# Optimization experiments

Hardware: AMD Instinct MI355X
Metric: run time of the kernel (lower is better)

Reference implementation:

```python
import jax, jax.numpy as jnp
import numpy as np

ITERATIONS = 5


def _dilate3x3(x):
    # 3x3 box 'conv' with all-ones kernel, padding=1 (SAME), single channel, NCHW
    k = jnp.ones((1, 1, 3, 3), x.dtype)
    return jax.lax.conv_general_dilated(
        x, k, window_strides=(1, 1), padding='SAME',
        dimension_numbers=('NCHW', 'OIHW', 'NCHW'))


def setup_inputs() -> dict:
    key = jax.random.key(0)
    k1, k2 = jax.random.split(key)
    H = W = 4096
    prediction = jax.random.uniform(k1, (1, 1, H, W), dtype=jnp.float32)
    ground_truth = jax.random.uniform(k2, (1, 1, H, W), dtype=jnp.float32)
    return {"prediction": prediction, "ground_truth": ground_truth}


def reference(prediction, ground_truth):
    # distance_weight = [1, 4, 9, 16, 25]
    weights = jnp.asarray([(i + 1) ** 2 for i in range(ITERATIONS)], dtype=jnp.float32)
    gt_sum = jnp.sum(ground_truth)
    fn_total = jnp.zeros((), dtype=jnp.float32)
    pred = prediction
    for i in range(ITERATIONS):  # fixed small unrolled loop (sequential recurrence)
        dilated = jnp.clip(_dilate3x3(pred), 0.0, 1.0)
        sharp = jax.nn.sigmoid(20.0 * (dilated - pred - 0.5))
        false_negative = ground_truth * sharp
        fn_total = fn_total + weights[i] * jnp.sum(false_negative) / gt_sum
        pred = pred + false_negative  # fed into next iteration's dilation
    return fn_total
```

## Files before the change

### kernel.cpp

```cpp
#include <hip/hip_runtime.h>

#define N 4096
#define CORE_W 116
#define NSTRIP 36
#define ROWS 36
#define NCHUNK 114
#define NSLOT 32
#define WPB 4
#define NBLOCK ((NSTRIP * NCHUNK) / WPB)


typedef float2 f2;
__device__ __forceinline__ f2 mkf2(float a, float b){ f2 r; r.x=a; r.y=b; return r; }

__device__ __forceinline__ f2 hsum(f2 v) {
    float m = v.x + v.y;
    float L = __shfl_up(v.y, 1);
    float R = __shfl_down(v.x, 1);
    return mkf2(L + m, m + R);
}

__device__ __forceinline__ f2 stepf(f2 p, f2 d, f2 g, f2* fn) {
    const float C1 = 28.853900817779268f;
    const float C2 = 14.426950408889634f;
    f2 o, f;
    {
        float dd = fminf(fmaxf(d.x, 0.f), 1.f);
        float u  = __builtin_fmaf(p.x - dd, C1, C2);
        float sh = __builtin_amdgcn_rcpf(1.f + __builtin_amdgcn_exp2f(u));
        f.x = g.x * sh; o.x = p.x + f.x;
    }
    {
        float dd = fminf(fmaxf(d.y, 0.f), 1.f);
        float u  = __builtin_fmaf(p.y - dd, C1, C2);
        float sh = __builtin_amdgcn_rcpf(1.f + __builtin_amdgcn_exp2f(u));
        f.y = g.y * sh; o.y = p.y + f.y;
    }
    *fn = f;
    return o;
}

__device__ __forceinline__ f2 ldrow(const float* __restrict__ base, int row,
                                    int gc, bool edge) {
    if (row < 0 || row >= N) return mkf2(0.f, 0.f);
    if (!edge) return *(const f2*)(base + (size_t)row * N + gc);
    float a = 0.f, b = 0.f;
    if (gc >= 0 && gc < N)         a = base[(size_t)row * N + gc];
    if (gc + 1 >= 0 && gc + 1 < N) b = base[(size_t)row * N + gc + 1];
    return mkf2(a, b);
}

__global__ __launch_bounds__(64 * WPB, 4) void wlc_main(
    const float* __restrict__ pred,
    const float* __restrict__ gt,
    float* __restrict__ ws)
{
    const int lane   = threadIdx.x & 63;
    const int wid    = threadIdx.x >> 6;
    const int linear = blockIdx.x * WPB + wid;
    const int strip  = linear % NSTRIP;
    const int chunk  = linear / NSTRIP;
    const int x0 = strip * CORE_W - 6;
    const int gc = x0 + 2 * lane;
    const bool edge = (strip == 0) || (strip == NSTRIP - 1);

    const int R0 = chunk * ROWS;
    const int R1 = min(R0 + ROWS, N);
    const int t0 = R0 - 5;
    const int t1 = R1 + 5;

    const float colm = (lane >= 3 && lane <= 60) ? 1.f : 0.f;
    const float m0 = (gc     < N) ? colm : 0.f;
    const float m1 = (gc + 1 < N) ? colm : 0.f;

    f2 pr[6], gb[6];
    f2 hp0, hp1, hp2, hp3, hp4;
    f2 ps0, ps1, ps2, ps3, ps4;
    f2 o1[2], o2[2], o3[2], o4[2];
#pragma unroll
    for (int i = 0; i < 6; ++i) { pr[i] = mkf2(0,0); gb[i] = mkf2(0,0); }
    hp0=hp1=hp2=hp3=hp4=mkf2(0,0);
    ps0=ps1=ps2=ps3=ps4=mkf2(0,0);
#pragma unroll
    for (int i = 0; i < 2; ++i) { o1[i]=o2[i]=o3[i]=o4[i]=mkf2(0,0); }

    pr[2] = ldrow(pred, t0,     gc, edge);
    pr[3] = ldrow(pred, t0 + 1, gc, edge);

    f2 swv = mkf2(0.f, 0.f);
    f2 gsv = mkf2(0.f, 0.f);

#define S6(o) ((8 + k + (o)) % 6)
#define S2(o) ((8 + k + (o)) % 2)

    for (int tb = t0; tb < t1; tb += 6) {
#pragma unroll
        for (int k = 0; k < 6; ++k) {
            const int t = tb + k;
            if (t < t1) {
                const f2 g5 = gb[S6(-5)];
                if (t + 2 <= R1 + 4) pr[S6(2)] = ldrow(pred, t + 2, gc, edge);
                if (t + 1 <= R1 + 3) gb[S6(1)] = ldrow(gt,   t + 1, gc, edge);

                const float w1 = (t-1 >= R0 && t-1 < R1) ? 1.f  : 0.f;
                const float w2 = (t-2 >= R0 && t-2 < R1) ? 4.f  : 0.f;
                const float w3 = (t-3 >= R0 && t-3 < R1) ? 9.f  : 0.f;
                const float w4 = (t-4 >= R0 && t-4 < R1) ? 16.f : 0.f;
                const bool  in5 = (t-5 >= R0 && t-5 < R1);
                const float w5 = in5 ? 25.f : 0.f;
                const float g1 = in5 ? 1.f  : 0.f;

                f2 hn, d, fn, o;

                hn = hsum(pr[S6(0)]);
                d  = mkf2(hn.x + ps0.x, hn.y + ps0.y);
                ps0 = mkf2(hn.x + hp0.x, hn.y + hp0.y);
                hp0 = hn;

                o = stepf(pr[S6(-1)], d, gb[S6(-1)], &fn);
                swv.x = __builtin_fmaf(w1, fn.x, swv.x);
                swv.y = __builtin_fmaf(w1, fn.y, swv.y);
                hn = hsum(o);  o1[S2(-1)] = o;
                d  = mkf2(hn.x + ps1.x, hn.y + ps1.y);
                ps1 = mkf2(hn.x + hp1.x, hn.y + hp1.y);
                hp1 = hn;

                o = stepf(o1[S2(-2)], d, gb[S6(-2)], &fn);
                swv.x = __builtin_fmaf(w2, fn.x, swv.x);
                swv.y = __builtin_fmaf(w2, fn.y, swv.y);
                hn = hsum(o);  o2[S2(-2)] = o;
                d  = mkf2(hn.x + ps2.x, hn.y + ps2.y);
                ps2 = mkf2(hn.x + hp2.x, hn.y + hp2.y);
                hp2 = hn;

                o = stepf(o2[S2(-3)], d, gb[S6(-3)], &fn);
                swv.x = __builtin_fmaf(w3, fn.x, swv.x);
                swv.y = __builtin_fmaf(w3, fn.y, swv.y);
                hn = hsum(o);  o3[S2(-3)] = o;
                d  = mkf2(hn.x + ps3.x, hn.y + ps3.y);
                ps3 = mkf2(hn.x + hp3.x, hn.y + hp3.y);
                hp3 = hn;

                o = stepf(o3[S2(-4)], d, gb[S6(-4)], &fn);
                swv.x = __builtin_fmaf(w4, fn.x, swv.x);
                swv.y = __builtin_fmaf(w4, fn.y, swv.y);
                hn = hsum(o);  o4[S2(-4)] = o;
                d  = mkf2(hn.x + ps4.x, hn.y + ps4.y);
                ps4 = mkf2(hn.x + hp4.x, hn.y + hp4.y);
                hp4 = hn;

                o = stepf(o4[S2(-5)], d, g5, &fn);
                swv.x = __builtin_fmaf(w5, fn.x, swv.x);
                swv.y = __builtin_fmaf(w5, fn.y, swv.y);
                gsv.x = __builtin_fmaf(g1, g5.x, gsv.x);
                gsv.y = __builtin_fmaf(g1, g5.y, gsv.y);
            }
        }
    }
#undef S6
#undef S2

    float vals[2];
    vals[0] = gsv.x * m0 + gsv.y * m1;
    vals[1] = swv.x * m0 + swv.y * m1;
    const int slot = (strip + chunk * NSTRIP) & (NSLOT - 1);
#pragma unroll
    for (int kk = 0; kk < 2; ++kk) {
        float v = vals[kk];
#pragma unroll
        for (int off = 32; off > 0; off >>= 1)
            v += __shfl_down(v, off, 64);
        if (lane == 0) atomicAdd(&ws[slot * 32 + kk], v);
    }
}

__global__ __launch_bounds__(64) void wlc_final(const float* __restrict__ ws,
                                                float* __restrict__ out)
{
    const int lane = threadIdx.x;
    float t0 = (lane < NSLOT) ? ws[lane * 32 + 0] : 0.f;
    float t1 = (lane < NSLOT) ? ws[lane * 32 + 1] : 0.f;
#pragma unroll
    for (int off = 32; off > 0; off >>= 1) {
        t0 += __shfl_down(t0, off, 64);
        t1 += __shfl_down(t1, off, 64);
    }
    if (lane == 0)
        out[0] = t1 / t0;
}

extern "C" void kernel_launch(void* const* d_in, const int* in_sizes, int n_in,
                              void* d_out, int out_size, void* d_ws, size_t ws_size,
                              hipStream_t stream)
{
    const float* pred = (const float*)d_in[0];
    const float* gtp  = (const float*)d_in[1];
    float* ws = (float*)d_ws;

    hipMemsetAsync(d_ws, 0, NSLOT * 32 * sizeof(float), stream);

    wlc_main<<<dim3(NBLOCK), 64 * WPB, 0, stream>>>(pred, gtp, ws);
    wlc_final<<<1, 64, 0, stream>>>(ws, (float*)d_out);
}
```

Before: 189.7 us.

## Skew stencil pipeline stages to break dependency chains and use larger row chunks

Restructures the five-iteration streaming stencil so that alternate stages lag by an extra row. Those stages can then compute their vertical sums from stored ring buffers instead of waiting on the stage just before them in the same row, which shortens the serial dependency chain per row. A second ground-truth stream is loaded at an offset to feed the delayed stages. Row chunks grow from 36 to 74 to amortise halo recompute, and the launch moves to single-wave blocks on a 2D grid. The cost is more registers, an extra gt load per row, and fewer waves in total (2016 vs 4104).

```diff
diff --git a/kernel.cpp b/kernel.cpp
--- a/kernel.cpp
+++ b/kernel.cpp
@@ -3,11 +3,9 @@
 #define N 4096
 #define CORE_W 116
 #define NSTRIP 36
-#define ROWS 36
-#define NCHUNK 114
+#define ROWS 74
+#define NCHUNK 56
 #define NSLOT 32
-#define WPB 4
-#define NBLOCK ((NSTRIP * NCHUNK) / WPB)
 
 
 typedef float2 f2;
@@ -50,115 +48,123 @@
     return mkf2(a, b);
 }
 
-__global__ __launch_bounds__(64 * WPB, 4) void wlc_main(
+__global__ __launch_bounds__(64, 2) void wlc_main(
     const float* __restrict__ pred,
     const float* __restrict__ gt,
     float* __restrict__ ws)
 {
-    const int lane   = threadIdx.x & 63;
-    const int wid    = threadIdx.x >> 6;
-    const int linear = blockIdx.x * WPB + wid;
-    const int strip  = linear % NSTRIP;
-    const int chunk  = linear / NSTRIP;
+    const int lane  = threadIdx.x;
+    const int strip = blockIdx.x;
+    const int chunk = blockIdx.y;
     const int x0 = strip * CORE_W - 6;
     const int gc = x0 + 2 * lane;
     const bool edge = (strip == 0) || (strip == NSTRIP - 1);
 
     const int R0 = chunk * ROWS;
     const int R1 = min(R0 + ROWS, N);
-    const int t0 = R0 - 5;
-    const int t1 = R1 + 5;
+    const int t0 = R0 - 6;
+    const int jmax = (R1 - R0) + 13;
 
     const float colm = (lane >= 3 && lane <= 60) ? 1.f : 0.f;
     const float m0 = (gc     < N) ? colm : 0.f;
     const float m1 = (gc + 1 < N) ? colm : 0.f;
 
-    f2 pr[6], gb[6];
-    f2 hp0, hp1, hp2, hp3, hp4;
-    f2 ps0, ps1, ps2, ps3, ps4;
-    f2 o1[2], o2[2], o3[2], o4[2];
-#pragma unroll
-    for (int i = 0; i < 6; ++i) { pr[i] = mkf2(0,0); gb[i] = mkf2(0,0); }
-    hp0=hp1=hp2=hp3=hp4=mkf2(0,0);
-    ps0=ps1=ps2=ps3=ps4=mkf2(0,0);
-#pragma unroll
-    for (int i = 0; i < 2; ++i) { o1[i]=o2[i]=o3[i]=o4[i]=mkf2(0,0); }
-
-    pr[2] = ldrow(pred, t0,     gc, edge);
-    pr[3] = ldrow(pred, t0 + 1, gc, edge);
+    f2 pr[4], gA[4], gB[6];
+    f2 h0r[3], h2r[3], h4r[3];
+    f2 hp1, ps1, hp3, ps3;
+    f2 o1r[2], o2r[3], o3r[2], o4r[3];
+#pragma unroll
+    for (int i = 0; i < 4; ++i) { pr[i] = mkf2(0,0); gA[i] = mkf2(0,0); }
+#pragma unroll
+    for (int i = 0; i < 6; ++i) gB[i] = mkf2(0,0);
+#pragma unroll
+    for (int i = 0; i < 3; ++i) { h0r[i]=h2r[i]=h4r[i]=mkf2(0,0);
+                                  o2r[i]=o4r[i]=mkf2(0,0); }
+    hp1=ps1=hp3=ps3=mkf2(0,0);
+    o1r[0]=o1r[1]=o3r[0]=o3r[1]=mkf2(0,0);
+
+    pr[0] = ldrow(pred, t0,     gc, edge);
+    pr[1] = ldrow(pred, t0 + 1, gc, edge);
 
     f2 swv = mkf2(0.f, 0.f);
     f2 gsv = mkf2(0.f, 0.f);
 
-#define S6(o) ((8 + k + (o)) % 6)
-#define S2(o) ((8 + k + (o)) % 2)
-
-    for (int tb = t0; tb < t1; tb += 6) {
-#pragma unroll
-        for (int k = 0; k < 6; ++k) {
-            const int t = tb + k;
-            if (t < t1) {
-                const f2 g5 = gb[S6(-5)];
-                if (t + 2 <= R1 + 4) pr[S6(2)] = ldrow(pred, t + 2, gc, edge);
-                if (t + 1 <= R1 + 3) gb[S6(1)] = ldrow(gt,   t + 1, gc, edge);
+#define M4(c) ((k + 16 + (c)) & 3)
+#define M3(c) ((k + 18 + (c)) % 3)
+#define M2(c) ((k + 16 + (c)) & 1)
+#define M6(c) ((k + 18 + (c)) % 6)
+
+    for (int jb = 0; jb < jmax; jb += 12) {
+#pragma unroll
+        for (int k = 0; k < 12; ++k) {
+            const int j = jb + k;
+            const int t = t0 + j;
+            if (j < jmax) {
+                if (t + 2 <= R1 + 4) pr[M4(2)] = ldrow(pred, t + 2, gc, edge);
+                if (t + 1 <= R1 + 3) gA[M4(1)] = ldrow(gt,   t + 1, gc, edge);
+                if (t     <= R1 + 4) gB[M6(3)] = ldrow(gt,   t - 3, gc, edge);
 
                 const float w1 = (t-1 >= R0 && t-1 < R1) ? 1.f  : 0.f;
                 const float w2 = (t-2 >= R0 && t-2 < R1) ? 4.f  : 0.f;
-                const float w3 = (t-3 >= R0 && t-3 < R1) ? 9.f  : 0.f;
-                const float w4 = (t-4 >= R0 && t-4 < R1) ? 16.f : 0.f;
-                const bool  in5 = (t-5 >= R0 && t-5 < R1);
+                const float w3 = (t-4 >= R0 && t-4 < R1) ? 9.f  : 0.f;
+                const float w4 = (t-5 >= R0 && t-5 < R1) ? 16.f : 0.f;
+                const bool  in5 = (t-7 >= R0 && t-7 < R1);
                 const float w5 = in5 ? 25.f : 0.f;
                 const float g1 = in5 ? 1.f  : 0.f;
 
-                f2 hn, d, fn, o;
-
-                hn = hsum(pr[S6(0)]);
-                d  = mkf2(hn.x + ps0.x, hn.y + ps0.y);
-                ps0 = mkf2(hn.x + hp0.x, hn.y + hp0.y);
-                hp0 = hn;
-
-                o = stepf(pr[S6(-1)], d, gb[S6(-1)], &fn);
+                const f2 d1 = mkf2(h0r[0].x+h0r[1].x+h0r[2].x, h0r[0].y+h0r[1].y+h0r[2].y);
+                const f2 d3 = mkf2(h2r[0].x+h2r[1].x+h2r[2].x, h2r[0].y+h2r[1].y+h2r[2].y);
+                const f2 d5 = mkf2(h4r[0].x+h4r[1].x+h4r[2].x, h4r[0].y+h4r[1].y+h4r[2].y);
+
+                f2 fn, o, hn;
+
+                h0r[M3(1)] = hsum(pr[M4(1)]);
+
+                o = stepf(pr[M4(3)], d1, gA[M4(3)], &fn);
                 swv.x = __builtin_fmaf(w1, fn.x, swv.x);
                 swv.y = __builtin_fmaf(w1, fn.y, swv.y);
-                hn = hsum(o);  o1[S2(-1)] = o;
-                d  = mkf2(hn.x + ps1.x, hn.y + ps1.y);
+                hn = hsum(o);
+                const f2 d2 = mkf2(hn.x + ps1.x, hn.y + ps1.y);
                 ps1 = mkf2(hn.x + hp1.x, hn.y + hp1.y);
                 hp1 = hn;
-
-                o = stepf(o1[S2(-2)], d, gb[S6(-2)], &fn);
+                o1r[M2(1)] = o;
+
+                o = stepf(o1r[M2(0)], d2, gA[M4(2)], &fn);
                 swv.x = __builtin_fmaf(w2, fn.x, swv.x);
                 swv.y = __builtin_fmaf(w2, fn.y, swv.y);
-                hn = hsum(o);  o2[S2(-2)] = o;
-                d  = mkf2(hn.x + ps2.x, hn.y + ps2.y);
-                ps2 = mkf2(hn.x + hp2.x, hn.y + hp2.y);
-                hp2 = hn;
-
-                o = stepf(o2[S2(-3)], d, gb[S6(-3)], &fn);
+                h2r[M3(1)] = hsum(o);
+                o2r[M3(1)] = o;
+
+                o = stepf(o2r[M3(2)], d3, gB[M6(2)], &fn);
                 swv.x = __builtin_fmaf(w3, fn.x, swv.x);
                 swv.y = __builtin_fmaf(w3, fn.y, swv.y);
-                hn = hsum(o);  o3[S2(-3)] = o;
-                d  = mkf2(hn.x + ps3.x, hn.y + ps3.y);
+                hn = hsum(o);
+                const f2 d4 = mkf2(hn.x + ps3.x, hn.y + ps3.y);
                 ps3 = mkf2(hn.x + hp3.x, hn.y + hp3.y);
                 hp3 = hn;
-
-                o = stepf(o3[S2(-4)], d, gb[S6(-4)], &fn);
+                o3r[M2(0)] = o;
+
+                o = stepf(o3r[M2(1)], d4, gB[M6(1)], &fn);
                 swv.x = __builtin_fmaf(w4, fn.x, swv.x);
                 swv.y = __builtin_fmaf(w4, fn.y, swv.y);
-                hn = hsum(o);  o4[S2(-4)] = o;
-                d  = mkf2(hn.x + ps4.x, hn.y + ps4.y);
-                ps4 = mkf2(hn.x + hp4.x, hn.y + hp4.y);
-                hp4 = hn;
-
-                o = stepf(o4[S2(-5)], d, g5, &fn);
-                swv.x = __builtin_fmaf(w5, fn.x, swv.x);
-                swv.y = __builtin_fmaf(w5, fn.y, swv.y);
-                gsv.x = __builtin_fmaf(g1, g5.x, gsv.x);
-                gsv.y = __builtin_fmaf(g1, g5.y, gsv.y);
+                h4r[M3(1)] = hsum(o);
+                o4r[M3(1)] = o;
+
+                {
+                    const f2 g5 = gB[M6(5)];
+                    o = stepf(o4r[M3(2)], d5, g5, &fn);
+                    swv.x = __builtin_fmaf(w5, fn.x, swv.x);
+                    swv.y = __builtin_fmaf(w5, fn.y, swv.y);
+                    gsv.x = __builtin_fmaf(g1, g5.x, gsv.x);
+                    gsv.y = __builtin_fmaf(g1, g5.y, gsv.y);
+                }
             }
         }
     }
-#undef S6
-#undef S2
+#undef M4
+#undef M3
+#undef M2
+#undef M6
 
     float vals[2];
     vals[0] = gsv.x * m0 + gsv.y * m1;
@@ -199,6 +205,6 @@
 
     hipMemsetAsync(d_ws, 0, NSLOT * 32 * sizeof(float), stream);
 
-    wlc_main<<<dim3(NBLOCK), 64 * WPB, 0, stream>>>(pred, gtp, ws);
+    wlc_main<<<dim3(NSTRIP, NCHUNK), 64, 0, stream>>>(pred, gtp, ws);
     wlc_final<<<1, 64, 0, stream>>>(ws, (float*)d_out);
 }
```

Measured after the change: 256.7 us. 1.35x slower.
